# Performance work log

Hardware: AMD Instinct MI355X
Metric: run time of the kernel (lower is better)

The kernel has to match this reference:

```python
import jax, jax.numpy as jnp
import numpy as np

B, L, D, H = 4, 2048, 1024, 16
DH = D // H
SCALE = DH ** -0.5


def setup_inputs() -> dict:
    key = jax.random.key(0)
    ks = jax.random.split(key, 8)
    q = jax.random.normal(ks[0], (B, L, D), dtype=jnp.float32)
    k = jax.random.normal(ks[1], (B, L, D), dtype=jnp.float32)
    v = jax.random.normal(ks[2], (B, L, D), dtype=jnp.float32)
    mask = jax.random.randint(ks[3], (B, 1, L), 0, 2, dtype=jnp.int32)
    s = D ** -0.5
    Wq = jax.random.normal(ks[4], (D, D), dtype=jnp.float32) * s
    Wk = jax.random.normal(ks[5], (D, D), dtype=jnp.float32) * s
    Wv = jax.random.normal(ks[6], (D, D), dtype=jnp.float32) * s
    Wo = jax.random.normal(ks[7], (D, D), dtype=jnp.float32) * s
    return {"q": q, "k": k, "v": v, "mask": mask, "Wq": Wq, "Wk": Wk, "Wv": Wv, "Wo": Wo}


def reference(q, k, v, mask, Wq, Wk, Wv, Wo):
    b, l, d = q.shape
    # torch Linear (no bias): x @ W^T; split heads -> [B, H, T, DH]
    qh = (q @ Wq.T).reshape(b, l, H, DH).transpose(0, 2, 1, 3)
    kh = (k @ Wk.T).reshape(b, -1, H, DH).transpose(0, 2, 1, 3)
    vh = (v @ Wv.T).reshape(b, -1, H, DH).transpose(0, 2, 1, 3)
    # scores [B, H, L, S]
    scores = jnp.einsum('bhld,bhsd->bhls', qh, kh) * SCALE
    scores = jnp.where(mask[:, None, :, :] != 1, jnp.float32(-1e9), scores)
    attn = jax.nn.softmax(scores, axis=-1)  # dropout defined but never applied in original forward
    out = jnp.einsum('bhls,bhsd->bhld', attn, vh)
    out = out.transpose(0, 2, 1, 3).reshape(b, l, d)
    return out @ Wo.T
```

## Files before the change

### kernel.cpp

```cpp
#include <hip/hip_runtime.h>
#include <cstddef>
#include <cstdint>

#define BB 4
#define LL 2048
#define DD 1024
#define HH 16
#define DHD 64
#define QSCALE 0.18033688f

typedef short s16x8 __attribute__((ext_vector_type(8)));
typedef short s16x4 __attribute__((ext_vector_type(4)));
typedef float f32x4 __attribute__((ext_vector_type(4)));
typedef unsigned int u32;
typedef u32 u32x2 __attribute__((ext_vector_type(2)));
typedef u32 u32x4 __attribute__((ext_vector_type(4)));

__device__ __forceinline__ short f2bf(float f) {
  union { float f; u32 u; } x; x.f = f;
  u32 r = x.u + 0x7FFFu + ((x.u >> 16) & 1u);
  return (short)(r >> 16);
}
__device__ __forceinline__ u32 pack2bf(float a, float b) {
  union { float f; u32 u; } x, y; x.f = a; y.f = b;
  return __builtin_amdgcn_perm(y.u + 0x8000u, x.u + 0x8000u, 0x07060302u);
}
__device__ __forceinline__ u32 cvtpk2bf(float lo, float hi) {
  u32 r;
  asm("v_cvt_pk_bf16_f32 %0, %1, %2" : "=v"(r) : "v"(lo), "v"(hi));
  return r;
}
__device__ __forceinline__ void gl2lds16(const short* g, short* l) {
  __builtin_amdgcn_global_load_lds(
      (const __attribute__((address_space(1))) unsigned int*)g,
      (__attribute__((address_space(3))) unsigned int*)l, 16, 0, 0);
}

__global__ __launch_bounds__(256) void prep_kernel(const float* __restrict__ q,
                                                   const float* __restrict__ k,
                                                   const float* __restrict__ v,
                                                   const float* __restrict__ Wq,
                                                   const float* __restrict__ Wk,
                                                   const float* __restrict__ Wv,
                                                   const float* __restrict__ Wo,
                                                   const int* __restrict__ mask,
                                                   short* __restrict__ qb,
                                                   short* __restrict__ kb,
                                                   short* __restrict__ vb,
                                                   short* __restrict__ Wqb,
                                                   short* __restrict__ Wkb,
                                                   short* __restrict__ Wvb,
                                                   short* __restrict__ Wob,
                                                   float* __restrict__ maskadd) {
  const int bb = blockIdx.x;
  if (bb < 24576) {
    const float* s; short* d;
    const int y = bb >> 13;
    if (y == 0) { s = q; d = qb; }
    else if (y == 1) { s = k; d = kb; }
    else { s = v; d = vb; }
    int i = (bb & 8191) * 256 + threadIdx.x;
    float4 x = ((const float4*)s)[i];
    s16x4 o; o.x = f2bf(x.x); o.y = f2bf(x.y); o.z = f2bf(x.z); o.w = f2bf(x.w);
    ((s16x4*)d)[i] = o;
  } else if (bb < 28672) {
    const int y = (bb - 24576) >> 10;
    const float* s; short* d; float sc = 1.0f;
    if (y == 0) { s = Wq; d = Wqb; sc = QSCALE; }
    else if (y == 1) { s = Wk; d = Wkb; }
    else if (y == 2) { s = Wv; d = Wvb; }
    else { s = Wo; d = Wob; }
    int i = ((bb - 24576) & 1023) * 256 + threadIdx.x;
    float4 x = ((const float4*)s)[i];
    s16x4 o; o.x = f2bf(x.x * sc); o.y = f2bf(x.y * sc); o.z = f2bf(x.z * sc); o.w = f2bf(x.w * sc);
    ((s16x4*)d)[i] = o;
  } else {
    int i = (bb - 28672) * 256 + threadIdx.x;
    int4 m = ((const int4*)mask)[i];
    f32x4 o;
    o[0] = (m.x == 1) ? 0.0f : -30000.0f;
    o[1] = (m.y == 1) ? 0.0f : -30000.0f;
    o[2] = (m.z == 1) ? 0.0f : -30000.0f;
    o[3] = (m.w == 1) ? 0.0f : -30000.0f;
    ((f32x4*)maskadd)[i] = o;
  }
}

__device__ __forceinline__ void gemm_core(const short* __restrict__ A, const short* __restrict__ B,
                                          int K, int bm, int bn, short* As, short* Bs,
                                          f32x4 (&acc)[4][4]) {
  const int tid = threadIdx.x;
  const int lane = tid & 63, wave = tid >> 6;
  const int wv = __builtin_amdgcn_readfirstlane(wave);
  const int quad = lane >> 4, l16 = lane & 15;
  const int wm = (wave >> 1) * 64, wn = (wave & 1) * 64;
  const short* ap[2]; const short* bp[2]; int lofs[2];
#pragma unroll
  for (int i = 0; i < 2; ++i) {
    int s = wv * 128 + i * 64 + lane;
    int r = s >> 2, c = s & 3;
    ap[i] = A + (size_t)(bm + r) * K + c * 8;
    bp[i] = B + (size_t)(bn + r) * K + c * 8;
    lofs[i] = s * 8;
  }
  const int rd = quad << 3;

#pragma unroll
  for (int i = 0; i < 2; ++i) gl2lds16(ap[i], &As[lofs[i]]);
#pragma unroll
  for (int i = 0; i < 2; ++i) gl2lds16(bp[i], &Bs[lofs[i]]);

  int cur = 0;
  for (int kk = 0; kk < K; kk += 32) {
    __syncthreads();
    if (kk + 32 < K) {
      const int nb = (cur ^ 1) * (128 * 32);
#pragma unroll
      for (int i = 0; i < 2; ++i) gl2lds16(ap[i] + kk + 32, &As[nb + lofs[i]]);
#pragma unroll
      for (int i = 0; i < 2; ++i) gl2lds16(bp[i] + kk + 32, &Bs[nb + lofs[i]]);
    }
    const short* Ac = &As[cur * (128 * 32)];
    const short* Bc = &Bs[cur * (128 * 32)];
    s16x8 af[4], bf[4];
#pragma unroll
    for (int t = 0; t < 4; ++t) af[t] = *(const s16x8*)&Ac[(wm + t * 16 + l16) * 32 + rd];
#pragma unroll
    for (int t = 0; t < 4; ++t) bf[t] = *(const s16x8*)&Bc[(wn + t * 16 + l16) * 32 + rd];
    __builtin_amdgcn_s_setprio(1);
#pragma unroll
    for (int mt = 0; mt < 4; ++mt)
#pragma unroll
      for (int nt = 0; nt < 4; ++nt)
        acc[mt][nt] = __builtin_amdgcn_mfma_f32_16x16x32_bf16(af[mt], bf[nt], acc[mt][nt], 0, 0, 0);
    __builtin_amdgcn_s_setprio(0);
    cur ^= 1;
  }
}

__global__ __launch_bounds__(256) void qkv_gemm(const short* __restrict__ qb, const short* __restrict__ kb,
                                                const short* __restrict__ vb, const short* __restrict__ Wqb,
                                                const short* __restrict__ Wkb, const short* __restrict__ Wvb,
                                                short* __restrict__ Qh, short* __restrict__ Kh,
                                                short* __restrict__ VT) {
  __shared__ short As[2 * 128 * 32];
  __shared__ short Bs[2 * 128 * 32];
  const int bid = blockIdx.x + ((blockIdx.y + (blockIdx.z << 6)) << 3);
  const int swz = (bid & 7) * 192 + (bid >> 3);
  const int bx = swz & 7, by = (swz >> 3) & 63, z = swz >> 9;
  const short *A, *B; short* C;
  if (z == 0) { A = qb; B = Wqb; C = Qh; }
  else if (z == 1) { A = kb; B = Wkb; C = Kh; }
  else { A = Wvb; B = vb; C = VT; }
  const int bm = (z == 2 ? bx : by) * 128;
  const int bn = (z == 2 ? by : bx) * 128;
  f32x4 acc[4][4] = {};
  gemm_core(A, B, DD, bm, bn, As, Bs, acc);

  const int lane = threadIdx.x & 63, wave = threadIdx.x >> 6;
  const int quad = lane >> 4, l16 = lane & 15;
  const int wm = (wave >> 1) * 64, wn = (wave & 1) * 64;
#pragma unroll
  for (int mt = 0; mt < 4; ++mt)
#pragma unroll
    for (int nt = 0; nt < 4; ++nt)
#pragma unroll
      for (int i = 0; i < 4; ++i) {
        int m = bm + wm + mt * 16 + quad * 4 + i;
        int n = bn + wn + nt * 16 + l16;
        float val = acc[mt][nt][i];
        if (z < 2) {
          int b = m >> 11, l = m & 2047;
          C[((size_t)(b * HH + (n >> 6)) << 17) + (size_t)l * DHD + (n & 63)] = f2bf(val);
        } else {
          int b = n >> 11, l = n & 2047;
          int loc = l & 63;
          int p = (loc & 0x23) | ((loc & 0x0C) << 1) | ((loc & 0x10) >> 2);
          C[((size_t)(b * DD + m) << 11) + (l & ~63) + p] = f2bf(val);
        }
      }
}

__global__ __launch_bounds__(256) void out_gemm(const short* __restrict__ A, const short* __restrict__ B,
                                                float* __restrict__ C) {
  __shared__ short As[2 * 128 * 32];
  __shared__ short Bs[2 * 128 * 32];
  const int bid = blockIdx.x + (blockIdx.y << 3);
  const int swz = (bid & 7) * 64 + (bid >> 3);
  const int bx = swz & 7, by = swz >> 3;
  const int bm = by * 128, bn = bx * 128;
  f32x4 acc[4][4] = {};
  gemm_core(A, B, DD, bm, bn, As, Bs, acc);
  const int lane = threadIdx.x & 63, wave = threadIdx.x >> 6;
  const int quad = lane >> 4, l16 = lane & 15;
  const int wm = (wave >> 1) * 64, wn = (wave & 1) * 64;
#pragma unroll
  for (int mt = 0; mt < 4; ++mt)
#pragma unroll
    for (int nt = 0; nt < 4; ++nt)
#pragma unroll
      for (int i = 0; i < 4; ++i) {
        int m = bm + wm + mt * 16 + quad * 4 + i;
        int n = bn + wn + nt * 16 + l16;
        C[(size_t)m * DD + n] = acc[mt][nt][i];
      }
}

__global__ __launch_bounds__(256, 4) void attn_kernel(const short* __restrict__ Qh,
                                                      const short* __restrict__ Kh,
                                                      const short* __restrict__ VT,
                                                      const float* __restrict__ maskadd,
                                                      short* __restrict__ AO) {
  __shared__ short Ks[2][64 * 64];
  __shared__ short Vs[2][64 * 64];
  const int tid  = threadIdx.x;
  const int lane = tid & 63, wave = tid >> 6;
  const int wv   = __builtin_amdgcn_readfirstlane(wave);
  const int quad = lane >> 4, l16 = lane & 15;
  const int a7 = l16 & 7;

  const int bid = blockIdx.x + (blockIdx.y << 4);
  const int swz = (bid & 7) * 128 + (bid >> 3);
  const int bx = swz & 15, bh = swz >> 4;
  const int b = bh >> 4;
  const int q0 = bx * 128;

  const float* mrow = maskadd + b * LL;
  const short* Qb = Qh + (size_t)bh * LL * DHD;
  const short* Kb = Kh + (size_t)bh * LL * DHD;
  const short* Vb = VT + (size_t)bh * DHD * LL;

  s16x8 qf[2][2];
#pragma unroll
  for (int u = 0; u < 2; ++u)
#pragma unroll
    for (int c = 0; c < 2; ++c)
      qf[u][c] = *(const s16x8*)&Qb[(size_t)(q0 + wv * 32 + u * 16 + l16) * DHD + c * 32 + quad * 8];

  const short* kp[2]; const short* vp[2]; int off[2];
#pragma unroll
  for (int t = 0; t < 2; ++t) {
    int s = wv * 128 + t * 64 + lane;
    int r = s >> 3, gl = (s & 7) ^ (r & 7);
    kp[t] = Kb + (size_t)r * DHD + gl * 8;
    vp[t] = Vb + (size_t)r * LL + gl * 8;
    off[t] = (wv * 128 + t * 64) * 8;
  }
  const int sw0 = (quad ^ a7) * 8;
  const int sw1 = ((4 + quad) ^ a7) * 8;

  s16x8 vone;
#pragma unroll
  for (int j = 0; j < 8; ++j) vone[j] = (short)0x3F80;

  f32x4 lsum[2] = {};
  f32x4 accO[2][4] = {};

#pragma unroll
  for (int t = 0; t < 2; ++t) gl2lds16(kp[t], &Ks[0][off[t]]);
#pragma unroll
  for (int t = 0; t < 2; ++t) gl2lds16(vp[t], &Vs[0][off[t]]);

  int cur = 0;
  for (int s0 = 0; s0 < LL; s0 += 64) {
    __syncthreads();
    if (s0 + 64 < LL) {
#pragma unroll
      for (int t = 0; t < 2; ++t) gl2lds16(kp[t] + (size_t)(s0 + 64) * DHD, &Ks[cur ^ 1][off[t]]);
#pragma unroll
      for (int t = 0; t < 2; ++t) gl2lds16(vp[t] + (s0 + 64), &Vs[cur ^ 1][off[t]]);
    }
    f32x4 mm[4];
#pragma unroll
    for (int st = 0; st < 4; ++st) mm[st] = *(const f32x4*)&mrow[s0 + st * 16 + quad * 4];

    const short* Kc = Ks[cur];
    const short* Vc = Vs[cur];
    s16x8 kf[4][2];
#pragma unroll
    for (int st = 0; st < 4; ++st) {
      kf[st][0] = *(const s16x8*)&Kc[(st * 16 + l16) * 64 + sw0];
      kf[st][1] = *(const s16x8*)&Kc[(st * 16 + l16) * 64 + sw1];
    }
    f32x4 sc[2][4];
#pragma unroll
    for (int u = 0; u < 2; ++u)
#pragma unroll
      for (int st = 0; st < 4; ++st) {
        sc[u][st] = __builtin_amdgcn_mfma_f32_16x16x32_bf16(kf[st][0], qf[u][0], mm[st], 0, 0, 0);
        sc[u][st] = __builtin_amdgcn_mfma_f32_16x16x32_bf16(kf[st][1], qf[u][1], sc[u][st], 0, 0, 0);
      }

    s16x8 pf[2][2];
#pragma unroll
    for (int u = 0; u < 2; ++u)
#pragma unroll
      for (int c = 0; c < 2; ++c) {
        union { u32x4 u4; s16x8 s8; } cv;
#pragma unroll
        for (int h = 0; h < 2; ++h) {
          const int st = 2 * c + h;
          float p0 = __builtin_amdgcn_exp2f(sc[u][st][0]);
          float p1 = __builtin_amdgcn_exp2f(sc[u][st][1]);
          float p2 = __builtin_amdgcn_exp2f(sc[u][st][2]);
          float p3 = __builtin_amdgcn_exp2f(sc[u][st][3]);
          cv.u4[h * 2 + 0] = cvtpk2bf(p0, p1);
          cv.u4[h * 2 + 1] = cvtpk2bf(p2, p3);
        }
        pf[u][c] = cv.s8;
      }

#pragma unroll
    for (int u = 0; u < 2; ++u) {
      lsum[u] = __builtin_amdgcn_mfma_f32_16x16x32_bf16(pf[u][0], vone, lsum[u], 0, 0, 0);
      lsum[u] = __builtin_amdgcn_mfma_f32_16x16x32_bf16(pf[u][1], vone, lsum[u], 0, 0, 0);
    }
#pragma unroll
    for (int dt = 0; dt < 4; ++dt) {
      const int drow = (dt * 16 + l16) * 64;
#pragma unroll
      for (int c = 0; c < 2; ++c) {
        s16x8 vf = *(const s16x8*)&Vc[drow + (((c * 4 + quad) ^ a7) << 3)];
#pragma unroll
        for (int u = 0; u < 2; ++u)
          accO[u][dt] = __builtin_amdgcn_mfma_f32_16x16x32_bf16(pf[u][c], vf, accO[u][dt], 0, 0, 0);
      }
    }
    cur ^= 1;
  }

  short* AOb = AO + (size_t)b * LL * DD + (size_t)(bh & 15) * DHD;
#pragma unroll
  for (int u = 0; u < 2; ++u) {
    f32x4 rl;
#pragma unroll
    for (int i = 0; i < 4; ++i) rl[i] = __builtin_amdgcn_rcpf(lsum[u][i]);
#pragma unroll
    for (int dt = 0; dt < 4; ++dt)
#pragma unroll
      for (int i = 0; i < 4; ++i) {
        int qr = q0 + wv * 32 + u * 16 + quad * 4 + i;
        AOb[(size_t)qr * DD + dt * 16 + l16] = f2bf(accO[u][dt][i] * rl[i]);
      }
  }
}

extern "C" void kernel_launch(void* const* d_in, const int* in_sizes, int n_in,
                              void* d_out, int out_size, void* d_ws, size_t ws_size,
                              hipStream_t stream) {
  const float* q   = (const float*)d_in[0];
  const float* k   = (const float*)d_in[1];
  const float* v   = (const float*)d_in[2];
  const int*  mask = (const int*)d_in[3];
  const float* Wq  = (const float*)d_in[4];
  const float* Wk  = (const float*)d_in[5];
  const float* Wv  = (const float*)d_in[6];
  const float* Wo  = (const float*)d_in[7];

  const size_t SX = (size_t)BB * LL * DD;
  const size_t SW = (size_t)DD * DD;
  short* w = (short*)d_ws;
  short* qb  = w;        short* kb  = qb + SX;  short* vb  = kb + SX;
  short* Wqb = vb + SX;  short* Wkb = Wqb + SW; short* Wvb = Wkb + SW; short* Wob = Wvb + SW;
  short* Qh  = Wob + SW; short* Kh  = Qh + SX;  short* VT  = Kh + SX;
  float* maskadd = (float*)(VT + SX);
  short* AO = qb;

  prep_kernel<<<28680, 256, 0, stream>>>(q, k, v, Wq, Wk, Wv, Wo, mask,
                                         qb, kb, vb, Wqb, Wkb, Wvb, Wob, maskadd);
  qkv_gemm<<<dim3(8, 64, 3), 256, 0, stream>>>(qb, kb, vb, Wqb, Wkb, Wvb, Qh, Kh, VT);
  attn_kernel<<<dim3(LL / 128, BB * HH), 256, 0, stream>>>(Qh, Kh, VT, maskadd, AO);
  out_gemm<<<dim3(8, 64), 256, 0, stream>>>(AO, Wob, (float*)d_out);
}
```

Baseline: 308.7 us.

## Fuse fp32-to-bf16 activation conversion into QKV GEMM tile loads

Removes the separate pass that converted q, k, v activations to bf16. The QKV GEMM now loads fp32 activation tiles into registers, converts them to bf16, and stores them to LDS after the MFMA block, which also prefetches the next tile. This avoids writing and rereading a bf16 copy of the activations. In exchange, each GEMM reads twice as many bytes per activation tile, and the register-staged path replaces async global-to-LDS loads, which may expose more load latency.

```diff
diff --git a/kernel.cpp b/kernel.cpp
--- a/kernel.cpp
+++ b/kernel.cpp
@@ -30,52 +30,42 @@
   asm("v_cvt_pk_bf16_f32 %0, %1, %2" : "=v"(r) : "v"(lo), "v"(hi));
   return r;
 }
+__device__ __forceinline__ s16x8 cvt8bf(const float4 a, const float4 b) {
+  union { u32x4 u; s16x8 s; } v;
+  v.u[0] = cvtpk2bf(a.x, a.y); v.u[1] = cvtpk2bf(a.z, a.w);
+  v.u[2] = cvtpk2bf(b.x, b.y); v.u[3] = cvtpk2bf(b.z, b.w);
+  return v.s;
+}
 __device__ __forceinline__ void gl2lds16(const short* g, short* l) {
   __builtin_amdgcn_global_load_lds(
       (const __attribute__((address_space(1))) unsigned int*)g,
       (__attribute__((address_space(3))) unsigned int*)l, 16, 0, 0);
 }
 
-__global__ __launch_bounds__(256) void prep_kernel(const float* __restrict__ q,
-                                                   const float* __restrict__ k,
-                                                   const float* __restrict__ v,
-                                                   const float* __restrict__ Wq,
+__global__ __launch_bounds__(256) void prep_kernel(const float* __restrict__ Wq,
                                                    const float* __restrict__ Wk,
                                                    const float* __restrict__ Wv,
                                                    const float* __restrict__ Wo,
                                                    const int* __restrict__ mask,
-                                                   short* __restrict__ qb,
-                                                   short* __restrict__ kb,
-                                                   short* __restrict__ vb,
                                                    short* __restrict__ Wqb,
                                                    short* __restrict__ Wkb,
                                                    short* __restrict__ Wvb,
                                                    short* __restrict__ Wob,
                                                    float* __restrict__ maskadd) {
   const int bb = blockIdx.x;
-  if (bb < 24576) {
-    const float* s; short* d;
-    const int y = bb >> 13;
-    if (y == 0) { s = q; d = qb; }
-    else if (y == 1) { s = k; d = kb; }
-    else { s = v; d = vb; }
-    int i = (bb & 8191) * 256 + threadIdx.x;
-    float4 x = ((const float4*)s)[i];
-    s16x4 o; o.x = f2bf(x.x); o.y = f2bf(x.y); o.z = f2bf(x.z); o.w = f2bf(x.w);
-    ((s16x4*)d)[i] = o;
-  } else if (bb < 28672) {
-    const int y = (bb - 24576) >> 10;
+  if (bb < 4096) {
+    const int y = bb >> 10;
     const float* s; short* d; float sc = 1.0f;
     if (y == 0) { s = Wq; d = Wqb; sc = QSCALE; }
     else if (y == 1) { s = Wk; d = Wkb; }
     else if (y == 2) { s = Wv; d = Wvb; }
     else { s = Wo; d = Wob; }
-    int i = ((bb - 24576) & 1023) * 256 + threadIdx.x;
+    int i = (bb & 1023) * 256 + threadIdx.x;
     float4 x = ((const float4*)s)[i];
     s16x4 o; o.x = f2bf(x.x * sc); o.y = f2bf(x.y * sc); o.z = f2bf(x.z * sc); o.w = f2bf(x.w * sc);
     ((s16x4*)d)[i] = o;
   } else {
-    int i = (bb - 28672) * 256 + threadIdx.x;
+    int i = (bb - 4096) * 256 + threadIdx.x;
     int4 m = ((const int4*)mask)[i];
     f32x4 o;
     o[0] = (m.x == 1) ? 0.0f : -30000.0f;
@@ -86,7 +76,9 @@
   }
 }
 
-__device__ __forceinline__ void gemm_core(const short* __restrict__ A, const short* __restrict__ B,
+template <int XMODE>
+__device__ __forceinline__ void gemm_core(const short* __restrict__ Abf, const short* __restrict__ Bbf,
+                                          const float* __restrict__ Afp, const float* __restrict__ Bfp,
                                           int K, int bm, int bn, short* As, short* Bs,
                                           f32x4 (&acc)[4][4]) {
   const int tid = threadIdx.x;
@@ -94,31 +86,47 @@
   const int wv = __builtin_amdgcn_readfirstlane(wave);
   const int quad = lane >> 4, l16 = lane & 15;
   const int wm = (wave >> 1) * 64, wn = (wave & 1) * 64;
-  const short* ap[2]; const short* bp[2]; int lofs[2];
+  const short* awp[2]; const short* bwp[2];
+  const float* axp[2]; const float* bxp[2];
+  int lofs[2];
 #pragma unroll
   for (int i = 0; i < 2; ++i) {
     int s = wv * 128 + i * 64 + lane;
     int r = s >> 2, c = s & 3;
-    ap[i] = A + (size_t)(bm + r) * K + c * 8;
-    bp[i] = B + (size_t)(bn + r) * K + c * 8;
     lofs[i] = s * 8;
+    if constexpr (XMODE == 1) axp[i] = Afp + (size_t)(bm + r) * K + c * 8;
+    else                      awp[i] = Abf + (size_t)(bm + r) * K + c * 8;
+    if constexpr (XMODE == 2) bxp[i] = Bfp + (size_t)(bn + r) * K + c * 8;
+    else                      bwp[i] = Bbf + (size_t)(bn + r) * K + c * 8;
   }
   const int rd = quad << 3;
 
-#pragma unroll
-  for (int i = 0; i < 2; ++i) gl2lds16(ap[i], &As[lofs[i]]);
-#pragma unroll
-  for (int i = 0; i < 2; ++i) gl2lds16(bp[i], &Bs[lofs[i]]);
+  float4 xr[2][2];
+#pragma unroll
+  for (int i = 0; i < 2; ++i) {
+    if constexpr (XMODE == 1) { xr[i][0] = ((const float4*)axp[i])[0]; xr[i][1] = ((const float4*)axp[i])[1]; }
+    else gl2lds16(awp[i], &As[lofs[i]]);
+    if constexpr (XMODE == 2) { xr[i][0] = ((const float4*)bxp[i])[0]; xr[i][1] = ((const float4*)bxp[i])[1]; }
+    else gl2lds16(bwp[i], &Bs[lofs[i]]);
+  }
+#pragma unroll
+  for (int i = 0; i < 2; ++i) {
+    if constexpr (XMODE == 1) *(s16x8*)&As[lofs[i]] = cvt8bf(xr[i][0], xr[i][1]);
+    if constexpr (XMODE == 2) *(s16x8*)&Bs[lofs[i]] = cvt8bf(xr[i][0], xr[i][1]);
+  }
 
   int cur = 0;
   for (int kk = 0; kk < K; kk += 32) {
     __syncthreads();
+    const int nb = (cur ^ 1) * (128 * 32);
     if (kk + 32 < K) {
-      const int nb = (cur ^ 1) * (128 * 32);
-#pragma unroll
-      for (int i = 0; i < 2; ++i) gl2lds16(ap[i] + kk + 32, &As[nb + lofs[i]]);
-#pragma unroll
-      for (int i = 0; i < 2; ++i) gl2lds16(bp[i] + kk + 32, &Bs[nb + lofs[i]]);
+#pragma unroll
+      for (int i = 0; i < 2; ++i) {
+        if constexpr (XMODE == 1) { xr[i][0] = ((const float4*)(axp[i] + kk + 32))[0]; xr[i][1] = ((const float4*)(axp[i] + kk + 32))[1]; }
+        else gl2lds16(awp[i] + kk + 32, &As[nb + lofs[i]]);
+        if constexpr (XMODE == 2) { xr[i][0] = ((const float4*)(bxp[i] + kk + 32))[0]; xr[i][1] = ((const float4*)(bxp[i] + kk + 32))[1]; }
+        else gl2lds16(bwp[i] + kk + 32, &Bs[nb + lofs[i]]);
+      }
     }
     const short* Ac = &As[cur * (128 * 32)];
     const short* Bc = &Bs[cur * (128 * 32)];
@@ -134,12 +142,19 @@
       for (int nt = 0; nt < 4; ++nt)
         acc[mt][nt] = __builtin_amdgcn_mfma_f32_16x16x32_bf16(af[mt], bf[nt], acc[mt][nt], 0, 0, 0);
     __builtin_amdgcn_s_setprio(0);
+    if (kk + 32 < K) {
+#pragma unroll
+      for (int i = 0; i < 2; ++i) {
+        if constexpr (XMODE == 1) *(s16x8*)&As[nb + lofs[i]] = cvt8bf(xr[i][0], xr[i][1]);
+        if constexpr (XMODE == 2) *(s16x8*)&Bs[nb + lofs[i]] = cvt8bf(xr[i][0], xr[i][1]);
+      }
+    }
     cur ^= 1;
   }
 }
 
-__global__ __launch_bounds__(256) void qkv_gemm(const short* __restrict__ qb, const short* __restrict__ kb,
-                                                const short* __restrict__ vb, const short* __restrict__ Wqb,
+__global__ __launch_bounds__(256) void qkv_gemm(const float* __restrict__ q, const float* __restrict__ k,
+                                                const float* __restrict__ v, const short* __restrict__ Wqb,
                                                 const short* __restrict__ Wkb, const short* __restrict__ Wvb,
                                                 short* __restrict__ Qh, short* __restrict__ Kh,
                                                 short* __restrict__ VT) {
@@ -148,14 +163,20 @@
   const int bid = blockIdx.x + ((blockIdx.y + (blockIdx.z << 6)) << 3);
   const int swz = (bid & 7) * 192 + (bid >> 3);
   const int bx = swz & 7, by = (swz >> 3) & 63, z = swz >> 9;
-  const short *A, *B; short* C;
-  if (z == 0) { A = qb; B = Wqb; C = Qh; }
-  else if (z == 1) { A = kb; B = Wkb; C = Kh; }
-  else { A = Wvb; B = vb; C = VT; }
+  f32x4 acc[4][4] = {};
   const int bm = (z == 2 ? bx : by) * 128;
   const int bn = (z == 2 ? by : bx) * 128;
-  f32x4 acc[4][4] = {};
-  gemm_core(A, B, DD, bm, bn, As, Bs, acc);
+  short* C;
+  if (z == 0) {
+    gemm_core<1>(nullptr, Wqb, q, nullptr, DD, bm, bn, As, Bs, acc);
+    C = Qh;
+  } else if (z == 1) {
+    gemm_core<1>(nullptr, Wkb, k, nullptr, DD, bm, bn, As, Bs, acc);
+    C = Kh;
+  } else {
+    gemm_core<2>(Wvb, nullptr, nullptr, v, DD, bm, bn, As, Bs, acc);
+    C = VT;
+  }
 
   const int lane = threadIdx.x & 63, wave = threadIdx.x >> 6;
   const int quad = lane >> 4, l16 = lane & 15;
@@ -190,7 +211,7 @@
   const int bx = swz & 7, by = swz >> 3;
   const int bm = by * 128, bn = bx * 128;
   f32x4 acc[4][4] = {};
-  gemm_core(A, B, DD, bm, bn, As, Bs, acc);
+  gemm_core<0>(A, B, nullptr, nullptr, DD, bm, bn, As, Bs, acc);
   const int lane = threadIdx.x & 63, wave = threadIdx.x >> 6;
   const int quad = lane >> 4, l16 = lane & 15;
   const int wm = (wave >> 1) * 64, wn = (wave & 1) * 64;
@@ -360,15 +381,14 @@
   const size_t SX = (size_t)BB * LL * DD;
   const size_t SW = (size_t)DD * DD;
   short* w = (short*)d_ws;
-  short* qb  = w;        short* kb  = qb + SX;  short* vb  = kb + SX;
-  short* Wqb = vb + SX;  short* Wkb = Wqb + SW; short* Wvb = Wkb + SW; short* Wob = Wvb + SW;
+  short* Wqb = w;        short* Wkb = Wqb + SW; short* Wvb = Wkb + SW; short* Wob = Wvb + SW;
   short* Qh  = Wob + SW; short* Kh  = Qh + SX;  short* VT  = Kh + SX;
   float* maskadd = (float*)(VT + SX);
-  short* AO = qb;
-
-  prep_kernel<<<28680, 256, 0, stream>>>(q, k, v, Wq, Wk, Wv, Wo, mask,
-                                         qb, kb, vb, Wqb, Wkb, Wvb, Wob, maskadd);
-  qkv_gemm<<<dim3(8, 64, 3), 256, 0, stream>>>(qb, kb, vb, Wqb, Wkb, Wvb, Qh, Kh, VT);
+  short* AO = (short*)(maskadd + (size_t)BB * LL);
+
+  prep_kernel<<<4104, 256, 0, stream>>>(Wq, Wk, Wv, Wo, mask,
+                                        Wqb, Wkb, Wvb, Wob, maskadd);
+  qkv_gemm<<<dim3(8, 64, 3), 256, 0, stream>>>(q, k, v, Wqb, Wkb, Wvb, Qh, Kh, VT);
   attn_kernel<<<dim3(LL / 128, BB * HH), 256, 0, stream>>>(Qh, Kh, VT, maskadd, AO);
   out_gemm<<<dim3(8, 64), 256, 0, stream>>>(AO, Wob, (float*)d_out);
 }
```

After: 370.0 us. 19.9% more time.
